# Optimization experiments

Measured on AMD Instinct MI355X. Metric: run time of the kernel, lower is better.

The kernel has to match this reference:

```python
import jax, jax.numpy as jnp
import numpy as np

# ---- quantization scales (per-tensor, as produced by from_float calibration) ----
IN_SCALE = 0.05      # ForwardTokenizer: fp32 hidden -> int8
ALPHA_Q = 1e-4       # W8A8B8O8 requant multipliers (already include 1/sqrt(head_dim) for q)
ALPHA_K = 1e-4
ALPHA_V = 1e-4
QK_ALPHA = 1e-3      # BMM_S8T_S8N_F32T dequant scale (q_scale * k_scale)
PV_ALPHA = 1.0/127.0 # BMM_S8T_S8N_S8T requant scale ((1/127)*v_scale/out_scale)
OUT_ALPHA = 1e-4     # W8A8BFP32OFP32 dequant scale
NUM_HEADS = 32


def _quant_i8(x, scale):
    # simulate int8 quantization in fp32 (values are exact small integers)
    return jnp.clip(jnp.round(x / scale), -128.0, 127.0)


def _w8a8b8o8(x_i8, W_i8, b_i8, alpha):
    # int8 GEMM with int8 bias, requantized to int8: clamp(round(alpha*(x@W^T) + b))
    acc = jnp.einsum('btd,ed->bte', x_i8, W_i8)  # int32 accumulator in fp32
    return jnp.clip(jnp.round(alpha * acc + b_i8), -128.0, 127.0)


def setup_inputs() -> dict:
    key = jax.random.key(0)
    ks = jax.random.split(key, 10)
    B, T, D = 2, 2048, 2560
    hidden_states = jax.random.normal(ks[0], (B, T, D), dtype=jnp.float32)
    # causal additive mask, shape (B,1,T,T)
    neg = jnp.float32(-1e9)
    causal = jnp.where(jnp.tril(jnp.ones((T, T), dtype=bool)), 0.0, neg)
    attention_mask = jnp.broadcast_to(causal[None, None], (B, 1, T, T)).astype(jnp.float32)
    # int8-valued weights/biases stored as fp32 integers in [-127,127]
    def i8(k, shape):
        return jax.random.randint(k, shape, -127, 128).astype(jnp.float32)
    Wq = i8(ks[1], (D, D)); bq = i8(ks[2], (D,))
    Wk = i8(ks[3], (D, D)); bk = i8(ks[4], (D,))
    Wv = i8(ks[5], (D, D)); bv = i8(ks[6], (D,))
    Wo = i8(ks[7], (D, D))
    bo = jax.random.normal(ks[8], (D,), dtype=jnp.float32) * 0.01  # fp32 out bias
    return {"hidden_states": hidden_states, "attention_mask": attention_mask,
            "Wq": Wq, "bq": bq, "Wk": Wk, "bk": bk, "Wv": Wv, "bv": bv,
            "Wo": Wo, "bo": bo}


def reference(hidden_states, attention_mask, Wq, bq, Wk, bk, Wv, bv, Wo, bo):
    B, T, D = hidden_states.shape
    H = NUM_HEADS
    Dh = D // H
    # ForwardTokenizer: fp32 -> int8
    x_i8 = _quant_i8(hidden_states, IN_SCALE)
    # fused int8 q/k/v projections (W8A8B8O8Linear)
    q = _w8a8b8o8(x_i8, Wq, bq, ALPHA_Q)
    k = _w8a8b8o8(x_i8, Wk, bk, ALPHA_K)
    v = _w8a8b8o8(x_i8, Wv, bv, ALPHA_V)
    # (B,T,D) -> (B,H,T,Dh)
    def shape(t):
        return t.reshape(B, T, H, Dh).transpose(0, 2, 1, 3)
    q, k, v = shape(q), shape(k), shape(v)
    # BMM_S8T_S8N_F32T: int8 q @ k^T dequantized to fp32
    attn_weights = QK_ALPHA * jnp.einsum('bhqd,bhkd->bhqk', q, k)
    attn_weights = attn_weights + attention_mask  # (B,H,T,T)
    attn_weights = jnp.maximum(attn_weights, jnp.finfo(jnp.float32).min)
    attn_probs = jax.nn.softmax(attn_weights, axis=-1)
    # requantize probs to int8: mul_(127).round_()
    p_i8 = jnp.round(attn_probs * 127.0)
    # BMM_S8T_S8N_S8T: int8 p @ v requantized to int8
    attn_out = jnp.clip(jnp.round(PV_ALPHA * jnp.einsum('bhqk,bhkd->bhqd', p_i8, v)), -128.0, 127.0)
    # (B,H,T,Dh) -> (B,T,D)
    attn_out = attn_out.transpose(0, 2, 1, 3).reshape(B, T, D)
    # W8A8BFP32OFP32Linear: int8 GEMM, fp32 dequant + fp32 bias
    out = OUT_ALPHA * jnp.einsum('btd,ed->bte', attn_out, Wo) + bo
    return out
```

## Files before the change

kernel.cpp:

```cpp
#include <hip/hip_runtime.h>
#include <stdint.h>

typedef int v4i __attribute__((ext_vector_type(4)));

#define MFMA_I8(a,b,c) __builtin_amdgcn_mfma_i32_16x16x64_i8(a,b,c,0,0,0)

#define TD 2560
#define TT 2048
#define TB 2
#define TH 32
#define TDH 80
#define TDHP 128
#define TM 4096

#define LOG2E_MS 1.4426950408889634e-3f
#define MASKI (-(1<<30))
#define MAGICF 12582912.0f

__device__ __forceinline__ float clamp8f(float v){ return fminf(fmaxf(v, -128.0f), 127.0f); }
__device__ __forceinline__ float fexp2(float x){ return __builtin_amdgcn_exp2f(x); }

__device__ __forceinline__ void gl_lds16(const int8_t* g, int8_t* l){
  __builtin_amdgcn_global_load_lds(
      (const __attribute__((address_space(1))) void*)g,
      (__attribute__((address_space(3))) void*)l, 16, 0, 0);
}

__global__ void k_quant(const float* __restrict__ x, int8_t* __restrict__ y, int n4){
  int stride = gridDim.x * blockDim.x;
  for (int i = blockIdx.x*blockDim.x + threadIdx.x; i < n4; i += stride){
    float4 v = ((const float4*)x)[i];
    char4 o;
    o.x = (int8_t)clamp8f(rintf(__fdiv_rn(v.x, 0.05f)));
    o.y = (int8_t)clamp8f(rintf(__fdiv_rn(v.y, 0.05f)));
    o.z = (int8_t)clamp8f(rintf(__fdiv_rn(v.z, 0.05f)));
    o.w = (int8_t)clamp8f(rintf(__fdiv_rn(v.w, 0.05f)));
    ((char4*)y)[i] = o;
  }
}

__global__ void k_conv4(const float* __restrict__ w0, const float* __restrict__ w1,
                        const float* __restrict__ w2, const float* __restrict__ w3,
                        int8_t* __restrict__ y0, int8_t* __restrict__ y1,
                        int8_t* __restrict__ y2, int8_t* __restrict__ y3, int n4){
  const int z = blockIdx.y;
  const float* w = z == 0 ? w0 : (z == 1 ? w1 : (z == 2 ? w2 : w3));
  int8_t* y = z == 0 ? y0 : (z == 1 ? y1 : (z == 2 ? y2 : y3));
  int stride = gridDim.x * blockDim.x;
  for (int i = blockIdx.x*blockDim.x + threadIdx.x; i < n4; i += stride){
    float4 v = ((const float4*)w)[i];
    char4 o;
    o.x = (int8_t)(int)rintf(v.x);
    o.y = (int8_t)(int)rintf(v.y);
    o.z = (int8_t)(int)rintf(v.z);
    o.w = (int8_t)(int)rintf(v.w);
    ((char4*)y)[i] = o;
  }
}

#define GB_SETUP                                                     \
  const int t = threadIdx.x;                                         \
  const int wv = t >> 6, l = t & 63, lhi = (l >> 4) & 3, llo = l & 15;\
  const int wr = wv >> 1, wc = wv & 1;                               \
  const int grow = t >> 3;                                           \
  const int gcol = ((t & 7) ^ ((t >> 3) & 7)) * 16;                  \
  const int sc0 = ((lhi ^ (llo & 7)) << 4);

#define GB_KLOOP(xsrc, wsrc)                                         \
  const int8_t* xa = (xsrc) + (size_t)(m0 + grow)*TD + gcol;         \
  const int8_t* wb = (wsrc) + (size_t)(n0 + grow)*TD + gcol;         \
  v4i acc[4][4] = {};                                                \
  for (int k0 = 0; k0 < TD; k0 += 128){                              \
    _Pragma("unroll")                                                \
    for (int i = 0; i < 4; ++i){                                     \
      gl_lds16(xa + (size_t)(i*32)*TD + k0, &As[(i*32 + wv*8)*128]); \
      gl_lds16(wb + (size_t)(i*32)*TD + k0, &Bs[(i*32 + wv*8)*128]); \
    }                                                                \
    __syncthreads();                                                 \
    v4i a[4][2], b[4][2];                                            \
    _Pragma("unroll")                                                \
    for (int mi = 0; mi < 4; ++mi){                                  \
      a[mi][0] = *(const v4i*)&As[(wr*64 + mi*16 + llo)*128 + sc0];  \
      a[mi][1] = *(const v4i*)&As[(wr*64 + mi*16 + llo)*128 + (sc0 ^ 64)];\
    }                                                                \
    _Pragma("unroll")                                                \
    for (int ni = 0; ni < 4; ++ni){                                  \
      b[ni][0] = *(const v4i*)&Bs[(wc*64 + ni*16 + llo)*128 + sc0];  \
      b[ni][1] = *(const v4i*)&Bs[(wc*64 + ni*16 + llo)*128 + (sc0 ^ 64)];\
    }                                                                \
    _Pragma("unroll")                                                \
    for (int mi = 0; mi < 4; ++mi)                                   \
      _Pragma("unroll")                                              \
      for (int ni = 0; ni < 4; ++ni){                                \
        acc[mi][ni] = MFMA_I8(a[mi][0], b[ni][0], acc[mi][ni]);      \
        acc[mi][ni] = MFMA_I8(a[mi][1], b[ni][1], acc[mi][ni]);      \
      }                                                              \
    __syncthreads();                                                 \
  }

__global__ __launch_bounds__(256) void k_qkvg(const int8_t* __restrict__ x,
    const int8_t* __restrict__ w0_, const int8_t* __restrict__ w1_, const int8_t* __restrict__ w2_,
    const float* __restrict__ b0_, const float* __restrict__ b1_, const float* __restrict__ b2_,
    int8_t* __restrict__ dq, int8_t* __restrict__ dk, int8_t* __restrict__ dv)
{
  __shared__ __align__(16) int8_t As[128*128];
  __shared__ __align__(16) int8_t Bs[128*128];
  const int z = blockIdx.z;
  const int8_t* w = z == 0 ? w0_ : (z == 1 ? w1_ : w2_);
  const float* bias = z == 0 ? b0_ : (z == 1 ? b1_ : b2_);
  const int m0 = blockIdx.x * 128, n0 = blockIdx.y * 128;
  GB_SETUP;
  GB_KLOOP(x, w);

  #pragma unroll
  for (int mi = 0; mi < 4; ++mi)
  #pragma unroll
  for (int ni = 0; ni < 4; ++ni)
  #pragma unroll
  for (int r = 0; r < 4; ++r){
    int rowg = m0 + wr*64 + mi*16 + lhi*4 + r;
    int colg = n0 + wc*64 + ni*16 + llo;
    float fv = __fadd_rn(__fmul_rn(1e-4f, (float)acc[mi][ni][r]), bias[colg]);
    int8_t q8 = (int8_t)clamp8f(rintf(fv));
    int bb = rowg >> 11, tl = rowg & 2047;
    int hh = colg / 80, dh = colg - hh*80;
    if (z == 0)      dq[((size_t)(bb*TH + hh)*TT + tl)*TDHP + dh] = q8;
    else if (z == 1) dk[((size_t)(bb*TH + hh)*TT + tl)*TDHP + dh] = q8;
    else             dv[((size_t)(bb*TH + hh)*TDH + dh)*TT + tl] = q8;
  }
}

#define OP_STAGE(bufi, k0) do{                                      \
    gl_lds16(xa0 + (k0), &As[bufi][(wv*16)*64]);                    \
    gl_lds16(xa1 + (k0), &As[bufi][(64 + wv*16)*64]);               \
    gl_lds16(wb0 + (k0), &Bs[bufi][(wv*16)*64]);                    \
    gl_lds16(wb1 + (k0), &Bs[bufi][(64 + wv*16)*64]); }while(0)

#define OP_COMP(bufi) do{                                           \
    v4i a[4], b[4];                                                 \
    _Pragma("unroll")                                               \
    for (int mi = 0; mi < 4; ++mi)                                  \
      a[mi] = *(const v4i*)&As[bufi][(wr*64 + mi*16 + llo)*64 + sca];\
    _Pragma("unroll")                                               \
    for (int ni = 0; ni < 4; ++ni)                                  \
      b[ni] = *(const v4i*)&Bs[bufi][(wc*64 + ni*16 + llo)*64 + sca];\
    _Pragma("unroll")                                               \
    for (int mi = 0; mi < 4; ++mi)                                  \
      _Pragma("unroll")                                             \
      for (int ni = 0; ni < 4; ++ni)                                \
        acc[mi][ni] = MFMA_I8(a[mi], b[ni], acc[mi][ni]); }while(0)

__global__ __launch_bounds__(256, 4) void k_oproj128(const int8_t* __restrict__ x,
    const int8_t* __restrict__ w, const float* __restrict__ bo,
    float* __restrict__ out)
{
  __shared__ __align__(16) int8_t As[2][128*64];
  __shared__ __align__(16) int8_t Bs[2][128*64];
  const int m0 = blockIdx.x * 128, n0 = blockIdx.y * 128;
  const int t = threadIdx.x;
  const int wv = t >> 6, l = t & 63, lhi = (l >> 4) & 3, llo = l & 15;
  const int wr = wv >> 1, wc = wv & 1;
  const int grow = l >> 2;
  const int gcol = ((l & 3) ^ ((l >> 3) & 3)) * 16;

  const int8_t* xa0 = x + (size_t)(m0 + wv*16 + grow)*TD + gcol;
  const int8_t* xa1 = x + (size_t)(m0 + 64 + wv*16 + grow)*TD + gcol;
  const int8_t* wb0 = w + (size_t)(n0 + wv*16 + grow)*TD + gcol;
  const int8_t* wb1 = w + (size_t)(n0 + 64 + wv*16 + grow)*TD + gcol;

  const int sca = (lhi ^ ((llo >> 1) & 3)) << 4;

  v4i acc[4][4] = {};
  OP_STAGE(0, 0);
  #pragma unroll 1
  for (int p = 0; p < 20; ++p){
    OP_STAGE(1, (2*p+1)*64);
    asm volatile("s_waitcnt vmcnt(4)" ::: "memory");
    __builtin_amdgcn_s_barrier();
    OP_COMP(0);
    __builtin_amdgcn_s_barrier();
    if (p < 19){
      OP_STAGE(0, (2*p+2)*64);
      asm volatile("s_waitcnt vmcnt(4)" ::: "memory");
    } else {
      asm volatile("s_waitcnt vmcnt(0)" ::: "memory");
    }
    __builtin_amdgcn_s_barrier();
    OP_COMP(1);
    __builtin_amdgcn_s_barrier();
  }

  #pragma unroll
  for (int mi = 0; mi < 4; ++mi)
  #pragma unroll
  for (int ni = 0; ni < 4; ++ni)
  #pragma unroll
  for (int r = 0; r < 4; ++r){
    int rowg = m0 + wr*64 + mi*16 + lhi*4 + r;
    int colg = n0 + wc*64 + ni*16 + llo;
    out[(size_t)rowg*TD + colg] =
        __fadd_rn(__fmul_rn(1e-4f, (float)acc[mi][ni][r]), bo[colg]);
  }
}

__global__ __launch_bounds__(256, 6) void k_attn6(const int8_t* __restrict__ qb_,
    const int8_t* __restrict__ kb_, const int8_t* __restrict__ vt_,
    int8_t* __restrict__ ao)
{
  __shared__ __align__(16) int8_t Ks[64*128];
  const int flat = blockIdx.x;
  const int g = flat & 7, ii = flat >> 3;
  const int qt = 31 - (ii >> 3);
  const int pair = g*8 + (ii & 7);
  const int h = pair & 31, b = pair >> 5;

  const int t = threadIdx.x, wv = t >> 6, l = t & 63, lhi = (l >> 4) & 3, llo = l & 15;
  const size_t bh = (size_t)(b*TH + h);
  const int8_t* qb = qb_ + bh*TT*TDHP;
  const int8_t* kb = kb_ + bh*TT*TDHP;
  const int8_t* vb = vt_ + bh*TDH*TT;

  const int qw0 = qt*64 + wv*16;
  const int qg = qw0 + llo;
  const int ktmax = qt + 1;

  int koff0[4], koff1[4];
  #pragma unroll
  for (int sub = 0; sub < 4; ++sub){
    const int row = sub*16 + llo, sw = row & 7;
    koff0[sub] = row*128 + (((lhi  ) ^ sw) << 4);
    koff1[sub] = row*128 + (((lhi+4) ^ sw) << 4);
  }

  v4i qa0 = *(const v4i*)(qb + (size_t)(qw0 + llo)*TDHP + lhi*16);
  v4i qa1 = {0,0,0,0};
  if (lhi == 0) qa1 = *(const v4i*)(qb + (size_t)(qw0 + llo)*TDHP + 64);

  const int srow = t >> 2, scp = (t & 3) * 2, ssw = srow & 7;
  const int8_t* kg = kb + (size_t)srow*TDHP + scp*16;
  int8_t* sdst0 = &Ks[srow*128 + (((scp  ) ^ ssw) << 4)];
  int8_t* sdst1 = &Ks[srow*128 + (((scp+1) ^ ssw) << 4)];

  int   M  = MASKI;
  float cm = __fmul_rn(LOG2E_MS, (float)MASKI);
  float ls = 0.0f;

  v4i pr0 = *(const v4i*)(kg);
  v4i pr1 = *(const v4i*)(kg + 16);
  *(v4i*)sdst0 = pr0; *(v4i*)sdst1 = pr1;
  for (int kt = 0; kt < ktmax; ++kt){
    if (kt + 1 < ktmax){
      pr0 = *(const v4i*)(kg + (size_t)(kt+1)*64*TDHP);
      pr1 = *(const v4i*)(kg + (size_t)(kt+1)*64*TDHP + 16);
    }
    __syncthreads();
    int sv[4][4];
    if (kt < qt){
      #pragma unroll
      for (int sub = 0; sub < 4; ++sub){
        v4i kf0 = *(const v4i*)&Ks[koff0[sub]];
        v4i kf1 = *(const v4i*)&Ks[koff1[sub]];
        v4i d = {}; d = MFMA_I8(kf0, qa0, d); d = MFMA_I8(kf1, qa1, d);
        sv[sub][0]=d[0]; sv[sub][1]=d[1]; sv[sub][2]=d[2]; sv[sub][3]=d[3];
      }
    } else {
      #pragma unroll
      for (int sub = 0; sub < 4; ++sub){
        if (sub <= wv){
          v4i kf0 = *(const v4i*)&Ks[koff0[sub]];
          v4i kf1 = *(const v4i*)&Ks[koff1[sub]];
          v4i d = {}; d = MFMA_I8(kf0, qa0, d); d = MFMA_I8(kf1, qa1, d);
          const int base = kt*64 + sub*16 + lhi*4;
          #pragma unroll
          for (int r = 0; r < 4; ++r)
            sv[sub][r] = (base + r <= qg) ? d[r] : MASKI;
        } else {
          #pragma unroll
          for (int r = 0; r < 4; ++r) sv[sub][r] = MASKI;
        }
      }
    }
    int m0 = max(max(sv[0][0], sv[0][1]), sv[0][2]);
    int m1 = max(max(sv[0][3], sv[1][0]), sv[1][1]);
    int m2 = max(max(sv[1][2], sv[1][3]), sv[2][0]);
    int m3 = max(max(sv[2][1], sv[2][2]), sv[2][3]);
    int m4 = max(max(sv[3][0], sv[3][1]), sv[3][2]);
    int tm = max(max(max(m0, m1), max(m2, m3)), max(m4, sv[3][3]));
    int Mn = max(M, tm);
    float cmN = __fmul_rn(LOG2E_MS, (float)Mn);
    float fac = fexp2(__fsub_rn(cm, cmN));
    float tot = 0.0f;
    #pragma unroll
    for (int sub = 0; sub < 4; ++sub){
      float e0 = fexp2(__fmaf_rn((float)sv[sub][0], LOG2E_MS, -cmN));
      float e1 = fexp2(__fmaf_rn((float)sv[sub][1], LOG2E_MS, -cmN));
      float e2 = fexp2(__fmaf_rn((float)sv[sub][2], LOG2E_MS, -cmN));
      float e3 = fexp2(__fmaf_rn((float)sv[sub][3], LOG2E_MS, -cmN));
      tot = __fadd_rn(tot, __fadd_rn(__fadd_rn(e0, e1), __fadd_rn(e2, e3)));
    }
    ls = __fmaf_rn(ls, fac, tot);
    M = Mn; cm = cmN;
    __syncthreads();
    if (kt + 1 < ktmax){ *(v4i*)sdst0 = pr0; *(v4i*)sdst1 = pr1; }
  }

  float rq;
  {
    float mm = cm, ll = ls;
    #pragma unroll
    for (int off = 16; off < 64; off <<= 1){
      float om = __shfl_xor(mm, off);
      float ol = __shfl_xor(ll, off);
      float mn = fmaxf(mm, om);
      ll = __fadd_rn(__fmul_rn(ll, fexp2(__fsub_rn(mm, mn))),
                     __fmul_rn(ol, fexp2(__fsub_rn(om, mn))));
      mm = mn;
    }
    cm = mm;
    rq = __fdiv_rn(127.0f, ll);
  }

  v4i pacc[5] = {};
  pr0 = *(const v4i*)(kg);
  pr1 = *(const v4i*)(kg + 16);
  __syncthreads();
  *(v4i*)sdst0 = pr0; *(v4i*)sdst1 = pr1;
  for (int kt = 0; kt < ktmax; ++kt){
    if (kt + 1 < ktmax){
      pr0 = *(const v4i*)(kg + (size_t)(kt+1)*64*TDHP);
      pr1 = *(const v4i*)(kg + (size_t)(kt+1)*64*TDHP + 16);
    }
    __syncthreads();
    uint32_t w[4] = {0u,0u,0u,0u};
    if (kt < qt){
      #pragma unroll
      for (int sub = 0; sub < 4; ++sub){
        v4i kf0 = *(const v4i*)&Ks[koff0[sub]];
        v4i kf1 = *(const v4i*)&Ks[koff1[sub]];
        v4i d = {}; d = MFMA_I8(kf0, qa0, d); d = MFMA_I8(kf1, qa1, d);
        uint32_t u0 = __float_as_uint(__fmaf_rn(fexp2(__fmaf_rn((float)d[0], LOG2E_MS, -cm)), rq, MAGICF));
        uint32_t u1 = __float_as_uint(__fmaf_rn(fexp2(__fmaf_rn((float)d[1], LOG2E_MS, -cm)), rq, MAGICF));
        uint32_t u2 = __float_as_uint(__fmaf_rn(fexp2(__fmaf_rn((float)d[2], LOG2E_MS, -cm)), rq, MAGICF));
        uint32_t u3 = __float_as_uint(__fmaf_rn(fexp2(__fmaf_rn((float)d[3], LOG2E_MS, -cm)), rq, MAGICF));
        w[sub] = (u0 & 0xffu) | ((u1 & 0xffu) << 8) | ((u2 & 0xffu) << 16) | (u3 << 24);
      }
    } else {
      #pragma unroll
      for (int sub = 0; sub < 4; ++sub){
        if (sub <= wv){
          v4i kf0 = *(const v4i*)&Ks[koff0[sub]];
          v4i kf1 = *(const v4i*)&Ks[koff1[sub]];
          v4i d = {}; d = MFMA_I8(kf0, qa0, d); d = MFMA_I8(kf1, qa1, d);
          const int base = kt*64 + sub*16 + lhi*4;
          uint32_t wrd = 0u;
          #pragma unroll
          for (int r = 0; r < 4; ++r){
            int sel = (base + r <= qg) ? d[r] : MASKI;
            uint32_t u = __float_as_uint(__fmaf_rn(fexp2(__fmaf_rn((float)sel, LOG2E_MS, -cm)), rq, MAGICF));
            wrd |= (u & 0xffu) << (8*r);
          }
          w[sub] = wrd;
        }
      }
    }
    #pragma unroll
    for (int bb = 0; bb < 2; ++bb){
      const int dist = 16 << bb;
      const int gb = (lhi >> bb) & 1;
      uint32_t nw[4];
      #pragma unroll
      for (int s = 0; s < 4; ++s){
        uint32_t tv = __shfl_xor(w[s ^ (1 << bb)], dist);
        nw[s] = (((s >> bb) & 1) == gb) ? w[s] : tv;
      }
      w[0]=nw[0]; w[1]=nw[1]; w[2]=nw[2]; w[3]=nw[3];
    }
    v4i pa;
    pa[0]=(int)w[0]; pa[1]=(int)w[1]; pa[2]=(int)w[2]; pa[3]=(int)w[3];
    #pragma unroll
    for (int dt = 0; dt < 5; ++dt){
      v4i vf = *(const v4i*)(vb + (size_t)(dt*16 + llo)*TT + kt*64 + lhi*16);
      pacc[dt] = MFMA_I8(vf, pa, pacc[dt]);
    }
    __syncthreads();
    if (kt + 1 < ktmax){ *(v4i*)sdst0 = pr0; *(v4i*)sdst1 = pr1; }
  }

  #pragma unroll
  for (int dt = 0; dt < 5; ++dt){
    uint32_t ob = 0u;
    #pragma unroll
    for (int r = 0; r < 4; ++r){
      int vq = (int)clamp8f(rintf(__fmul_rn((float)pacc[dt][r], (float)(1.0/127.0))));
      ob |= ((uint32_t)(uint8_t)(int8_t)vq) << (8*r);
    }
    *(uint32_t*)(ao + ((size_t)(b*TT) + qw0 + llo)*TD + h*TDH + dt*16 + lhi*4) = ob;
  }
}

extern "C" void kernel_launch(void* const* d_in, const int* in_sizes, int n_in,
                              void* d_out, int out_size, void* d_ws, size_t ws_size,
                              hipStream_t stream) {
  const float* hidden = (const float*)d_in[0];
  const float* Wq = (const float*)d_in[2];
  const float* bq = (const float*)d_in[3];
  const float* Wk = (const float*)d_in[4];
  const float* bk = (const float*)d_in[5];
  const float* Wv = (const float*)d_in[6];
  const float* bv = (const float*)d_in[7];
  const float* Wo = (const float*)d_in[8];
  const float* bo = (const float*)d_in[9];
  float* out = (float*)d_out;

  char* ws = (char*)d_ws;
  const size_t SZ_X  = (size_t)TM * TD;
  const size_t SZ_W  = (size_t)TD * TD;
  const size_t SZ_QK = (size_t)TB * TH * TT * TDHP;
  const size_t SZ_V  = (size_t)TB * TH * TDH * TT;
  int8_t* x8   = (int8_t*)ws;
  int8_t* wq8  = (int8_t*)(ws + SZ_X);
  int8_t* wk8  = wq8 + SZ_W;
  int8_t* wv8  = wk8 + SZ_W;
  int8_t* wo8  = wv8 + SZ_W;
  int8_t* qpad = wo8 + SZ_W;
  int8_t* kpad = qpad + SZ_QK;
  int8_t* vt   = kpad + SZ_QK;
  int8_t* ao   = vt + SZ_V;

  k_quant<<<4096, 256, 0, stream>>>(hidden, x8, (int)(SZ_X/4));
  k_conv4<<<dim3(1024, 4), 256, 0, stream>>>(Wq, Wk, Wv, Wo, wq8, wk8, wv8, wo8, (int)(SZ_W/4));

  k_qkvg<<<dim3(TM/128, TD/128, 3), 256, 0, stream>>>(x8, wq8, wk8, wv8, bq, bk, bv,
                                                      qpad, kpad, vt);

  k_attn6<<<dim3(2048), 256, 0, stream>>>(qpad, kpad, vt, ao);

  k_oproj128<<<dim3(TM/128, TD/128), 256, 0, stream>>>(ao, wo8, bo, out);
}
```

Before: 308.4 us.

## Double-buffer QKV GEMM K-loop with async global-to-LDS prefetch

```diff
diff --git a/kernel.cpp b/kernel.cpp
--- a/kernel.cpp
+++ b/kernel.cpp
@@ -58,59 +58,87 @@
   }
 }
 
-#define GB_SETUP                                                     \
-  const int t = threadIdx.x;                                         \
-  const int wv = t >> 6, l = t & 63, lhi = (l >> 4) & 3, llo = l & 15;\
-  const int wr = wv >> 1, wc = wv & 1;                               \
-  const int grow = t >> 3;                                           \
-  const int gcol = ((t & 7) ^ ((t >> 3) & 7)) * 16;                  \
-  const int sc0 = ((lhi ^ (llo & 7)) << 4);
-
-#define GB_KLOOP(xsrc, wsrc)                                         \
-  const int8_t* xa = (xsrc) + (size_t)(m0 + grow)*TD + gcol;         \
-  const int8_t* wb = (wsrc) + (size_t)(n0 + grow)*TD + gcol;         \
-  v4i acc[4][4] = {};                                                \
-  for (int k0 = 0; k0 < TD; k0 += 128){                              \
-    _Pragma("unroll")                                                \
-    for (int i = 0; i < 4; ++i){                                     \
-      gl_lds16(xa + (size_t)(i*32)*TD + k0, &As[(i*32 + wv*8)*128]); \
-      gl_lds16(wb + (size_t)(i*32)*TD + k0, &Bs[(i*32 + wv*8)*128]); \
-    }                                                                \
-    __syncthreads();                                                 \
-    v4i a[4][2], b[4][2];                                            \
-    _Pragma("unroll")                                                \
-    for (int mi = 0; mi < 4; ++mi){                                  \
-      a[mi][0] = *(const v4i*)&As[(wr*64 + mi*16 + llo)*128 + sc0];  \
-      a[mi][1] = *(const v4i*)&As[(wr*64 + mi*16 + llo)*128 + (sc0 ^ 64)];\
-    }                                                                \
-    _Pragma("unroll")                                                \
-    for (int ni = 0; ni < 4; ++ni){                                  \
-      b[ni][0] = *(const v4i*)&Bs[(wc*64 + ni*16 + llo)*128 + sc0];  \
-      b[ni][1] = *(const v4i*)&Bs[(wc*64 + ni*16 + llo)*128 + (sc0 ^ 64)];\
-    }                                                                \
-    _Pragma("unroll")                                                \
-    for (int mi = 0; mi < 4; ++mi)                                   \
-      _Pragma("unroll")                                              \
-      for (int ni = 0; ni < 4; ++ni){                                \
-        acc[mi][ni] = MFMA_I8(a[mi][0], b[ni][0], acc[mi][ni]);      \
-        acc[mi][ni] = MFMA_I8(a[mi][1], b[ni][1], acc[mi][ni]);      \
-      }                                                              \
-    __syncthreads();                                                 \
-  }
-
 __global__ __launch_bounds__(256) void k_qkvg(const int8_t* __restrict__ x,
     const int8_t* __restrict__ w0_, const int8_t* __restrict__ w1_, const int8_t* __restrict__ w2_,
     const float* __restrict__ b0_, const float* __restrict__ b1_, const float* __restrict__ b2_,
     int8_t* __restrict__ dq, int8_t* __restrict__ dk, int8_t* __restrict__ dv)
 {
-  __shared__ __align__(16) int8_t As[128*128];
-  __shared__ __align__(16) int8_t Bs[128*128];
+  __shared__ __align__(16) int8_t Ah[2][2][128*64];
+  __shared__ __align__(16) int8_t Bh[2][2][128*64];
   const int z = blockIdx.z;
   const int8_t* w = z == 0 ? w0_ : (z == 1 ? w1_ : w2_);
   const float* bias = z == 0 ? b0_ : (z == 1 ? b1_ : b2_);
   const int m0 = blockIdx.x * 128, n0 = blockIdx.y * 128;
-  GB_SETUP;
-  GB_KLOOP(x, w);
+  const int t = threadIdx.x;
+  const int wv = t >> 6, l = t & 63, lhi = (l >> 4) & 3, llo = l & 15;
+  const int wr = wv >> 1, wc = wv & 1;
+
+  const int grow0 = wv*16 + (l >> 2);
+  const int scl = ((l & 3) ^ ((l >> 2) & 3)) * 16;
+  const int8_t* xa = x + (size_t)(m0 + grow0)*TD + scl;
+  const int8_t* wb = w + (size_t)(n0 + grow0)*TD + scl;
+
+  const int fo = ((lhi ^ (llo & 3)) << 4);
+
+#define STG(buf, kh, kt) do{                                         \
+    const int kofs = (kt)*128 + (kh)*64;                             \
+    gl_lds16(xa + kofs,                 &Ah[buf][kh][(wv*16)*64]);   \
+    gl_lds16(xa + (size_t)64*TD + kofs, &Ah[buf][kh][(64+wv*16)*64]);\
+    gl_lds16(wb + kofs,                 &Bh[buf][kh][(wv*16)*64]);   \
+    gl_lds16(wb + (size_t)64*TD + kofs, &Bh[buf][kh][(64+wv*16)*64]);\
+  }while(0)
+
+#define CMP(buf, kh) do{                                             \
+    v4i a[4], bfr[4];                                                \
+    _Pragma("unroll")                                                \
+    for (int mi = 0; mi < 4; ++mi)                                   \
+      a[mi] = *(const v4i*)&Ah[buf][kh][(wr*64 + mi*16 + llo)*64 + fo];\
+    _Pragma("unroll")                                                \
+    for (int ni = 0; ni < 4; ++ni)                                   \
+      bfr[ni] = *(const v4i*)&Bh[buf][kh][(wc*64 + ni*16 + llo)*64 + fo];\
+    _Pragma("unroll")                                                \
+    for (int mi = 0; mi < 4; ++mi)                                   \
+      _Pragma("unroll")                                              \
+      for (int ni = 0; ni < 4; ++ni)                                 \
+        acc[mi][ni] = MFMA_I8(a[mi], bfr[ni], acc[mi][ni]);          \
+  }while(0)
+
+  v4i acc[4][4] = {};
+
+  STG(0, 0, 0);
+  STG(0, 1, 0);
+
+  #pragma unroll 1
+  for (int kt = 0; kt < 19; ++kt){
+    const int b = kt & 1;
+    STG(b ^ 1, 0, kt + 1);
+    asm volatile("s_waitcnt vmcnt(8)" ::: "memory");
+    __builtin_amdgcn_s_barrier();
+    __builtin_amdgcn_sched_barrier(0);
+    CMP(b, 0);
+    __builtin_amdgcn_sched_barrier(0);
+    __builtin_amdgcn_s_barrier();
+    STG(b ^ 1, 1, kt + 1);
+    asm volatile("s_waitcnt vmcnt(8)" ::: "memory");
+    __builtin_amdgcn_s_barrier();
+    __builtin_amdgcn_sched_barrier(0);
+    CMP(b, 1);
+    __builtin_amdgcn_sched_barrier(0);
+    __builtin_amdgcn_s_barrier();
+  }
+  asm volatile("s_waitcnt vmcnt(4)" ::: "memory");
+  __builtin_amdgcn_s_barrier();
+  __builtin_amdgcn_sched_barrier(0);
+  CMP(1, 0);
+  __builtin_amdgcn_sched_barrier(0);
+  __builtin_amdgcn_s_barrier();
+  asm volatile("s_waitcnt vmcnt(0)" ::: "memory");
+  __builtin_amdgcn_s_barrier();
+  __builtin_amdgcn_sched_barrier(0);
+  CMP(1, 1);
+
+#undef STG
+#undef CMP
 
   #pragma unroll
   for (int mi = 0; mi < 4; ++mi)
```

New measurement: 327.7 us. +6.3%, slower.
